# Performance work log

Measured on AMD Instinct MI355X. Metric: run time of the kernel, lower is better.

Reference implementation:

```python
import jax, jax.numpy as jnp
import numpy as np

NV, NK, DK, DV, KC = 32, 16, 128, 128, 4  # value heads, key heads, head dims, conv kernel
EPS = 1e-6


def setup_inputs() -> dict:
    key = jax.random.key(0)
    ks = jax.random.split(key, 10)
    B, T, D = 2, 4096, 2048
    key_dim, value_dim = NK * DK, NV * DV
    conv_dim = 2 * key_dim + value_dim
    s = 0.02
    return {
        "hidden_states": jax.random.normal(ks[0], (B, T, D), jnp.float32),
        "W_qkv": jax.random.normal(ks[1], (D, conv_dim), jnp.float32) * s,
        "W_z": jax.random.normal(ks[2], (D, value_dim), jnp.float32) * s,
        "W_b": jax.random.normal(ks[3], (D, NV), jnp.float32) * s,
        "W_a": jax.random.normal(ks[4], (D, NV), jnp.float32) * s,
        "conv_w": jax.random.normal(ks[5], (conv_dim, KC), jnp.float32) * 0.2,
        "dt_bias": jnp.ones((NV,), jnp.float32),
        "A_log": jnp.log(jax.random.uniform(ks[6], (NV,), jnp.float32, 0.5, 16.0)),
        "norm_w": jnp.ones((DV,), jnp.float32),
        "W_out": jax.random.normal(ks[7], (value_dim, D), jnp.float32) * s,
    }


def _silu(x):
    return x * jax.nn.sigmoid(x)


def _l2norm(x):
    return x * jax.lax.rsqrt(jnp.sum(x * x, axis=-1, keepdims=True) + EPS)


def _gated_delta_rule(q, k, v, g, beta):
    # q,k: [B,T,H,DK]; v: [B,T,H,DV]; g,beta: [B,T,H]
    tm = lambda x: jnp.moveaxis(x, 1, 0)  # time-major
    B, T, H = q.shape[0], q.shape[1], q.shape[2]
    S0 = jnp.zeros((B, H, q.shape[-1], v.shape[-1]), q.dtype)

    def step(S, xs):
        qt, kt, vt, gt, bt = xs
        S = S * jnp.exp(gt)[..., None, None]                       # decay
        kS = jnp.einsum('bhk,bhkv->bhv', kt, S)                    # k^T S
        S = S + bt[..., None, None] * kt[..., :, None] * (vt - kS)[..., None, :]
        o = jnp.einsum('bhk,bhkv->bhv', qt, S)
        return S, o

    _, o = jax.lax.scan(step, S0, (tm(q), tm(k), tm(v), tm(g), tm(beta)))
    return jnp.moveaxis(o, 0, 1)  # [B,T,H,DV]


def reference(hidden_states, W_qkv, W_z, W_b, W_a, conv_w, dt_bias, A_log, norm_w, W_out):
    B, T, D = hidden_states.shape
    key_dim, value_dim = NK * DK, NV * DV

    mixed = hidden_states @ W_qkv                                  # [B,T,conv_dim]
    z = (hidden_states @ W_z).reshape(B, T, NV, DV)
    beta = jax.nn.sigmoid(hidden_states @ W_b)                     # [B,T,NV]
    a = hidden_states @ W_a
    g = -jnp.exp(A_log) * jax.nn.softplus(a + dt_bias)             # [B,T,NV]

    # causal depthwise short conv (kernel KC) + silu
    xp = jnp.pad(mixed, ((0, 0), (KC - 1, 0), (0, 0)))
    conv = sum(xp[:, i:i + T, :] * conv_w[:, i] for i in range(KC))
    mixed = _silu(conv)

    q, k, v = jnp.split(mixed, [key_dim, 2 * key_dim], axis=-1)
    q = q.reshape(B, T, NK, DK)
    k = k.reshape(B, T, NK, DK)
    v = v.reshape(B, T, NV, DV)
    rep = NV // NK
    q = jnp.repeat(q, rep, axis=2)
    k = jnp.repeat(k, rep, axis=2)

    q = _l2norm(q) * (DK ** -0.5)
    k = _l2norm(k)

    o = _gated_delta_rule(q, k, v, g, beta)                        # [B,T,NV,DV]

    # fused gated RMSNorm: rmsnorm(o)*w * silu(z)
    var = jnp.mean(o * o, axis=-1, keepdims=True)
    o = o * jax.lax.rsqrt(var + 1e-6) * norm_w * _silu(z)

    return o.reshape(B, T, value_dim) @ W_out
```

## Files before the change

kernel.cpp:

```cpp
#include <hip/hip_runtime.h>
#include <hip/hip_bf16.h>


typedef __attribute__((ext_vector_type(8))) short short8;
typedef __attribute__((ext_vector_type(4))) float f32x4;
typedef unsigned short us;

static __device__ __forceinline__ us f2b(float f) {
  __hip_bfloat16 h = __float2bfloat16(f);
  return __builtin_bit_cast(us, h);
}
static __device__ __forceinline__ float b2f(us u) {
  return __bfloat162float(__builtin_bit_cast(__hip_bfloat16, u));
}
static __device__ __forceinline__ void bar_lds() {
  asm volatile("s_waitcnt lgkmcnt(0)" ::: "memory");
  __builtin_amdgcn_s_barrier();
}

__global__ __launch_bounds__(256) void cvt_f32_bf16(const float* __restrict__ in,
    us* __restrict__ out, long n4) {
  long i = (long)blockIdx.x * 256 + threadIdx.x;
  long stride = (long)gridDim.x * 256;
  for (; i < n4; i += stride) {
    float4 f = reinterpret_cast<const float4*>(in)[i];
    ushort4 u;
    u.x = f2b(f.x); u.y = f2b(f.y); u.z = f2b(f.z); u.w = f2b(f.w);
    reinterpret_cast<ushort4*>(out)[i] = u;
  }
}

__global__ __launch_bounds__(256) void transpose_cvt(const float* __restrict__ in,
    us* __restrict__ out, int K, int N, int Nfull, int coloff, int row_off) {
  __shared__ float tile[64][65];
  int tid = threadIdx.x;
  int n0 = blockIdx.x * 64, k0 = blockIdx.y * 64;
  int tx = tid & 15, ty = tid >> 4;
#pragma unroll
  for (int r = 0; r < 4; ++r) {
    int kk = k0 + ty + r * 16, nn = n0 + tx * 4;
    float4 v = make_float4(0.f, 0.f, 0.f, 0.f);
    if (kk < K && nn < N)
      v = *reinterpret_cast<const float4*>(in + (size_t)kk * Nfull + coloff + nn);
    tile[ty + r * 16][tx * 4 + 0] = v.x;
    tile[ty + r * 16][tx * 4 + 1] = v.y;
    tile[ty + r * 16][tx * 4 + 2] = v.z;
    tile[ty + r * 16][tx * 4 + 3] = v.w;
  }
  __syncthreads();
#pragma unroll
  for (int g = 0; g < 2; ++g) {
    int s = tid + g * 256;
    int nn = s >> 3, ks = (s & 7) * 8;
    if (n0 + nn < N && k0 + ks < K) {
      us ov[8];
#pragma unroll
      for (int i = 0; i < 8; ++i) ov[i] = f2b(tile[ks + i][nn]);
      *reinterpret_cast<uint4*>(out + (size_t)(n0 + nn + row_off) * K + k0 + ks) =
          *reinterpret_cast<uint4*>(ov);
    }
  }
}

template <bool BF16OUT>
__global__ __launch_bounds__(512, 1) void gemm256(const us* __restrict__ A,
    const us* __restrict__ B, void* __restrict__ Cout, int K, int ldC) {
  __shared__ us Abuf[2][256 * 64];
  __shared__ us Bbuf[2][256 * 64];
  int tid = threadIdx.x, w = tid >> 6, lane = tid & 63;
  int wr = w >> 2, wc = w & 3;
  int fr = lane & 15, j4 = lane >> 4;
  int lin = blockIdx.y * gridDim.x + blockIdx.x;
  int nwg = gridDim.x * gridDim.y;
  int wg = (lin & 7) * (nwg >> 3) + (lin >> 3);
  int bx = wg % gridDim.x, by = wg / gridDim.x;
  size_t bm = (size_t)bx * 256, bn = (size_t)by * 256;

  const us *aG[4], *bG[4];
  us *aL[2][4], *bL[2][4];
#pragma unroll
  for (int u = 0; u < 4; ++u) {
    int idx = u * 512 + tid;
    int row = idx >> 3, sl = idx & 7;
    int sg = (sl ^ (row & 7)) * 8;
    aG[u] = A + (bm + row) * K + sg;
    bG[u] = B + (bn + row) * K + sg;
    int lbase = (u * 64 + w * 8) * 64;
#pragma unroll
    for (int bf = 0; bf < 2; ++bf) {
      aL[bf][u] = &Abuf[bf][lbase];
      bL[bf][u] = &Bbuf[bf][lbase];
    }
  }

  f32x4 acc[8][4] = {};
#pragma unroll
  for (int u = 0; u < 4; ++u) {
    __builtin_amdgcn_global_load_lds((const void*)aG[u], (void*)aL[0][u], 16, 0, 0);
    __builtin_amdgcn_global_load_lds((const void*)bG[u], (void*)bL[0][u], 16, 0, 0);
  }
  __syncthreads();

  int nt = K >> 6;
  for (int t = 0; t < nt; ++t) {
    int cur = t & 1, nxt = cur ^ 1;
    const us* Ac = Abuf[cur];
    const us* Bc = Bbuf[cur];
    int kt1 = (t + 1) << 6;
    bool more = (t + 1 < nt);
#pragma unroll
    for (int q = 0; q < 4; ++q) {
      if (more) {
        __builtin_amdgcn_global_load_lds((const void*)(aG[q] + kt1), (void*)aL[nxt][q], 16, 0, 0);
        __builtin_amdgcn_global_load_lds((const void*)(bG[q] + kt1), (void*)bL[nxt][q], 16, 0, 0);
      }
      short8 a0[2], a1[2], bfv[4][2];
      int Ra0 = wr * 128 + 2 * q * 16 + fr;
      int Ra1 = Ra0 + 16;
#pragma unroll
      for (int ks = 0; ks < 2; ++ks) {
        a0[ks] = *reinterpret_cast<const short8*>(&Ac[Ra0 * 64 + (((ks * 4 + j4) ^ (Ra0 & 7)) * 8)]);
        a1[ks] = *reinterpret_cast<const short8*>(&Ac[Ra1 * 64 + (((ks * 4 + j4) ^ (Ra1 & 7)) * 8)]);
#pragma unroll
        for (int fj = 0; fj < 4; ++fj) {
          int Rb = wc * 64 + fj * 16 + fr;
          bfv[fj][ks] = *reinterpret_cast<const short8*>(&Bc[Rb * 64 + (((ks * 4 + j4) ^ (Rb & 7)) * 8)]);
        }
      }
      __builtin_amdgcn_s_setprio(1);
#pragma unroll
      for (int ks = 0; ks < 2; ++ks)
#pragma unroll
        for (int fj = 0; fj < 4; ++fj) {
          acc[2 * q][fj] = __builtin_amdgcn_mfma_f32_16x16x32_bf16(a0[ks], bfv[fj][ks], acc[2 * q][fj], 0, 0, 0);
          acc[2 * q + 1][fj] = __builtin_amdgcn_mfma_f32_16x16x32_bf16(a1[ks], bfv[fj][ks], acc[2 * q + 1][fj], 0, 0, 0);
        }
      __builtin_amdgcn_s_setprio(0);
    }
    __syncthreads();
  }
#pragma unroll
  for (int fi = 0; fi < 8; ++fi)
#pragma unroll
    for (int fj = 0; fj < 4; ++fj) {
      size_t col = bn + wc * 64 + fj * 16 + fr;
#pragma unroll
      for (int e = 0; e < 4; ++e) {
        size_t r = bm + wr * 128 + fi * 16 + j4 * 4 + e;
        size_t off = r * ldC + col;
        if (BF16OUT) reinterpret_cast<us*>(Cout)[off] = f2b(acc[fi][fj][e]);
        else reinterpret_cast<float*>(Cout)[off] = acc[fi][fj][e];
      }
    }
}

__global__ __launch_bounds__(256) void gemm_lds_f32(const us* __restrict__ A,
    const us* __restrict__ B, float* __restrict__ Cout,
    int K, int Nb1, int Nvalid, int ldC) {
  __shared__ us Ash[128 * 64];
  __shared__ us Bsh[128 * 64];
  int tid = threadIdx.x, w = tid >> 6, lane = tid & 63;
  int bm = blockIdx.x * 128, bn = blockIdx.y * 128;
  int wm = (w >> 1) * 64, wn = (w & 1) * 64;
  const us* aP[4]; const us* bP[4]; us* lA[4]; us* lB[4];
#pragma unroll
  for (int i = 0; i < 4; ++i) {
    int idx = i * 256 + tid;
    int row = idx >> 3;
    int sg = ((idx & 7) ^ (row & 7)) * 8;
    aP[i] = A + (size_t)(bm + row) * K + sg;
    int rb = bn + row; if (rb > Nb1) rb = Nb1;
    bP[i] = B + (size_t)rb * K + sg;
    lA[i] = &Ash[(i * 256 + w * 64) * 8];
    lB[i] = &Bsh[(i * 256 + w * 64) * 8];
  }
  f32x4 acc[4][4] = {};
  int fr = lane & 15, j = lane >> 4;
  for (int kt = 0; kt < K; kt += 64) {
#pragma unroll
    for (int i = 0; i < 4; ++i)
      __builtin_amdgcn_global_load_lds((const void*)(aP[i] + kt), (void*)lA[i], 16, 0, 0);
#pragma unroll
    for (int i = 0; i < 4; ++i)
      __builtin_amdgcn_global_load_lds((const void*)(bP[i] + kt), (void*)lB[i], 16, 0, 0);
    __syncthreads();
#pragma unroll
    for (int ks = 0; ks < 2; ++ks) {
      short8 af[4], bfr[4];
#pragma unroll
      for (int f = 0; f < 4; ++f) {
        int Ra = wm + f * 16 + fr;
        af[f] = *reinterpret_cast<const short8*>(&Ash[Ra * 64 + (((ks * 4 + j) ^ (Ra & 7)) * 8)]);
        int Rb = wn + f * 16 + fr;
        bfr[f] = *reinterpret_cast<const short8*>(&Bsh[Rb * 64 + (((ks * 4 + j) ^ (Rb & 7)) * 8)]);
      }
#pragma unroll
      for (int i = 0; i < 4; ++i)
#pragma unroll
        for (int jj = 0; jj < 4; ++jj)
          acc[i][jj] = __builtin_amdgcn_mfma_f32_16x16x32_bf16(af[i], bfr[jj], acc[i][jj], 0, 0, 0);
    }
    __syncthreads();
  }
#pragma unroll
  for (int i = 0; i < 4; ++i)
#pragma unroll
    for (int jj = 0; jj < 4; ++jj) {
      int c0 = bn + wn + jj * 16 + (lane & 15);
      if (c0 < Nvalid) {
#pragma unroll
        for (int e = 0; e < 4; ++e) {
          int r = bm + wm + i * 16 + (lane >> 4) * 4 + e;
          Cout[(size_t)r * ldC + c0] = acc[i][jj][e];
        }
      }
    }
}

template <int MODE>
__global__ __launch_bounds__(256) void conv_chunk(const us* __restrict__ mixed,
    const float* __restrict__ cw, us* __restrict__ outp, int headbase) {
  int bp = blockIdx.x, b = bp >> 10, tloc = (bp & 1023) * 4, tid = threadIdx.x;
  int c0 = tid * 8;
  float wv[8][4];
#pragma unroll
  for (int jj = 0; jj < 8; ++jj) {
    float4 w4 = *reinterpret_cast<const float4*>(cw + (size_t)(c0 + jj) * 4);
    wv[jj][0] = w4.x; wv[jj][1] = w4.y; wv[jj][2] = w4.z; wv[jj][3] = w4.w;
  }
  us rw[7][8];
#pragma unroll
  for (int i = 0; i < 7; ++i) {
    int tt = tloc - 3 + i;
    if (tt >= 0 && tt < 4096)
      *reinterpret_cast<uint4*>(rw[i]) = *reinterpret_cast<const uint4*>(
          mixed + ((size_t)(b * 4096 + tt)) * 2048 + c0);
    else
      *reinterpret_cast<uint4*>(rw[i]) = make_uint4(0, 0, 0, 0);
  }
  float x[4][8];
#pragma unroll
  for (int jj = 0; jj < 8; ++jj) {
#pragma unroll
    for (int tk = 0; tk < 4; ++tk) {
      float a = 0.f;
#pragma unroll
      for (int i = 0; i < 4; ++i) a += b2f(rw[tk + i][jj]) * wv[jj][i];
      x[tk][jj] = a / (1.f + __expf(-a));
    }
  }
  size_t bt0 = (size_t)b * 4096 + tloc;
  us ov[8];
  if (MODE < 2) {
    float s[4] = {};
#pragma unroll
    for (int tk = 0; tk < 4; ++tk) {
#pragma unroll
      for (int jj = 0; jj < 8; ++jj) s[tk] += x[tk][jj] * x[tk][jj];
    }
#pragma unroll
    for (int m = 1; m < 16; m <<= 1) {
#pragma unroll
      for (int tk = 0; tk < 4; ++tk) s[tk] += __shfl_xor(s[tk], m, 64);
    }
    const float sc = (MODE == 0 ? 0.08838834764831845f : 1.f);
    int head = tid >> 4, d0 = c0 & 127;
#pragma unroll
    for (int tk = 0; tk < 4; ++tk) {
      float rn = rsqrtf(s[tk] + 1e-6f) * sc;
#pragma unroll
      for (int jj = 0; jj < 8; ++jj) ov[jj] = f2b(x[tk][jj] * rn);
      *reinterpret_cast<uint4*>(outp + ((bt0 + tk) * 16 + head) * 128 + d0) =
          *reinterpret_cast<uint4*>(ov);
    }
  } else {
    int head = headbase + (c0 >> 7), d0 = c0 & 127;
#pragma unroll
    for (int tk = 0; tk < 4; ++tk) {
#pragma unroll
      for (int jj = 0; jj < 8; ++jj) ov[jj] = f2b(x[tk][jj]);
      *reinterpret_cast<uint4*>(outp + ((bt0 + tk) * 32 + head) * 128 + d0) =
          *reinterpret_cast<uint4*>(ov);
    }
  }
}

__global__ __launch_bounds__(256) void gates_cumsum(const float* __restrict__ ba,
    const float* __restrict__ dt_bias, const float* __restrict__ A_log,
    float* __restrict__ bl_g, float* __restrict__ beta_g) {
  int widx = blockIdx.x * 4 + (threadIdx.x >> 6);
  int lane = threadIdx.x & 63;
  int bh = widx >> 6, chunk = widx & 63;
  int b = bh >> 5, h = bh & 31;
  size_t btl = (size_t)b * 4096 + chunk * 64 + lane;
  float bv = ba[btl * 64 + h];
  float av = ba[btl * 64 + 32 + h];
  float beta = 1.f / (1.f + __expf(-bv));
  float xx = av + dt_bias[h];
  float sp = (xx > 20.f) ? xx : log1pf(__expf(xx));
  float g = -__expf(A_log[h]) * sp;
#pragma unroll
  for (int off = 1; off < 64; off <<= 1) {
    float n = __shfl_up(g, off, 64);
    if (lane >= off) g += n;
  }
  bl_g[(size_t)widx * 64 + lane] = g;
  beta_g[(size_t)widx * 64 + lane] = beta;
}

static __device__ __forceinline__ f32x4 tile_range(const us* A, int lda,
    const us* B, int ldb, int rt, int ct, int l0, int nk, int lane, f32x4 acc) {
  const us* ar = A + (rt * 16 + (lane & 15)) * lda + l0 * 16 + (lane >> 4) * 8;
  const us* br = B + (ct * 16 + (lane & 15)) * ldb + l0 * 16 + (lane >> 4) * 8;
#pragma unroll
  for (int ks = 0; ks < nk; ++ks) {
    short8 a = *reinterpret_cast<const short8*>(ar + ks * 32);
    short8 bb = *reinterpret_cast<const short8*>(br + ks * 32);
    acc = __builtin_amdgcn_mfma_f32_16x16x32_bf16(a, bb, acc, 0, 0, 0);
  }
  return acc;
}
template <int SA, int SB>
static __device__ __forceinline__ f32x4 tile_swz(const us* A, int lda,
    const us* B, int ldb, int rt, int ct, int nk, int lane, f32x4 acc) {
  int ra = rt * 16 + (lane & 15);
  int rb = ct * 16 + (lane & 15);
  int j = lane >> 4;
#pragma unroll
  for (int ks = 0; ks < nk; ++ks) {
    int slot = j + 4 * ks;
    int oa = (SA >= 0) ? ((slot ^ ((ra >> (SA < 0 ? 0 : SA)) & 7)) * 8) : (slot * 8);
    int ob = (SB >= 0) ? ((slot ^ ((rb >> (SB < 0 ? 0 : SB)) & 7)) * 8) : (slot * 8);
    short8 a = *reinterpret_cast<const short8*>(A + ra * lda + oa);
    short8 bb = *reinterpret_cast<const short8*>(B + rb * ldb + ob);
    acc = __builtin_amdgcn_mfma_f32_16x16x32_bf16(a, bb, acc, 0, 0, 0);
  }
  return acc;
}

__global__ __launch_bounds__(512, 1) void scan_p1(
    const us* __restrict__ k, const float* __restrict__ bl_g,
    const float* __restrict__ beta_g, us* __restrict__ Tg) {
  __shared__ us Kb[64 * 136];
  __shared__ us Ebt[64 * 72];
  __shared__ us W1[64 * 72], W1t[64 * 72], W3[64 * 72];
  __shared__ float bl_s[64], bet_s[64];
  us* const Eb = Kb;

  int bid = blockIdx.x, bh = bid >> 6, c = bid & 63;
  int b = bh >> 5, h = bh & 31, hk = h >> 1;
  int tid = threadIdx.x, w = tid >> 6, lane = tid & 63;
  int row = tid >> 3, c16 = (tid & 7) * 16;
  size_t bt0 = (size_t)b * 4096 + c * 64;

  const int TR_[10] = {0, 1, 1, 2, 2, 2, 3, 3, 3, 3};
  const int TC_[10] = {0, 0, 1, 0, 1, 2, 0, 1, 2, 3};

  const us* kp = k + ((bt0 + row) * 16 + hk) * 128 + c16;
  uint4 kr0 = reinterpret_cast<const uint4*>(kp)[0];
  uint4 kr1 = reinterpret_cast<const uint4*>(kp)[1];
  int gbase = (bh * 64 + c) * 64;
  if (tid < 64) { bl_s[tid] = bl_g[gbase + tid]; bet_s[tid] = beta_g[gbase + tid]; }
  *reinterpret_cast<uint4*>(&Kb[row * 136 + c16]) = kr0;
  *reinterpret_cast<uint4*>(&Kb[row * 136 + c16 + 8]) = kr1;
  __syncthreads();
  {
    int art = w & 3;
#pragma unroll
    for (int s = 0; s < 2; ++s) {
      int ct = (w >> 2) * 2 + s;
      f32x4 a = tile_range(Kb, 136, Kb, 136, art, ct, 0, 4, lane, f32x4{});
#pragma unroll
      for (int e = 0; e < 4; ++e) {
        int tr = art * 16 + (lane >> 4) * 4 + e;
        int cl = ct * 16 + (lane & 15);
        float dv = (cl < tr) ? bet_s[tr] * __expf(bl_s[tr] - bl_s[cl]) * a[e] : 0.f;
        W1[tr * 72 + cl] = f2b(dv);
        W1t[cl * 72 + tr] = f2b(dv);
        W3[tr * 72 + cl] = f2b((tr == cl ? 1.f : 0.f) - dv);
      }
    }
  }
  __syncthreads();
  f32x4 freg[2] = {};
#pragma unroll
  for (int it = 1; it <= 5; ++it) {
    if (it > 1) {
#pragma unroll
      for (int s = 0; s < 2; ++s) {
        int j = w + s * 8;
        if (j < 10) {
          int r = TR_[j], cc0 = TC_[j];
#pragma unroll
          for (int e = 0; e < 4; ++e) {
            int rr = r * 16 + (lane >> 4) * 4 + e, cl = cc0 * 16 + (lane & 15);
            W3[rr * 72 + cl] = f2b(b2f(W3[rr * 72 + cl]) + freg[s][e]);
          }
        }
      }
    }
    if (it == 1) {
      const int ZR[12] = {0, 0, 0, 1, 1, 2, 1, 2, 2, 3, 3, 3};
      const int ZC[12] = {1, 2, 3, 2, 3, 3, 0, 0, 1, 0, 1, 2};
#pragma unroll
      for (int u = 0; u < 12; ++u) {
        if ((u & 7) != w) continue;
        us* arr = (u < 6) ? Eb : Ebt;
        if (lane < 32) {
          int rr = ZR[u] * 16 + (lane >> 1);
          *reinterpret_cast<uint4*>(&arr[rr * 72 + ZC[u] * 16 + (lane & 1) * 8]) =
              make_uint4(0, 0, 0, 0);
        }
      }
    }
    const us* Es  = (it & 1) ? W1  : Eb;
    const us* Est = (it & 1) ? W1t : Ebt;
    us* Ed  = (it & 1) ? Eb  : W1;
    us* Edt = (it & 1) ? Ebt : W1t;
#pragma unroll
    for (int s = 0; s < 2; ++s) {
      int j = w + s * 8;
      if (j < 10) {
        int r = TR_[j], cc0 = TC_[j];
        int l0 = cc0 & ~1, nk = (r - l0 + 2) >> 1;
        f32x4 a = tile_range(Es, 72, Est, 72, r, cc0, l0, nk, lane, f32x4{});
#pragma unroll
        for (int e = 0; e < 4; ++e) {
          int rr = r * 16 + (lane >> 4) * 4 + e, cl = cc0 * 16 + (lane & 15);
          us val = f2b(a[e]);
          Ed[rr * 72 + cl] = val;
          Edt[cl * 72 + rr] = val;
        }
      }
    }
    __syncthreads();
    const us* Ent = (it & 1) ? Ebt : W1t;
#pragma unroll
    for (int s = 0; s < 2; ++s) {
      int j = w + s * 8;
      if (j < 10) {
        int r = TR_[j], cc0 = TC_[j];
        int l0 = cc0 & ~1, nk = (r - l0 + 2) >> 1;
        freg[s] = tile_range(W3, 72, Ent, 72, r, cc0, l0, nk, lane, f32x4{});
      }
    }
    __syncthreads();
  }
#pragma unroll
  for (int s = 0; s < 2; ++s) {
    int j = w + s * 8;
    if (j < 10) {
      int r = TR_[j], cc0 = TC_[j];
#pragma unroll
      for (int e = 0; e < 4; ++e) {
        int rr = r * 16 + (lane >> 4) * 4 + e, cl = cc0 * 16 + (lane & 15);
        W3[rr * 72 + cl] = f2b(b2f(W3[rr * 72 + cl]) + freg[s][e]);
      }
    }
  }
  __syncthreads();
  *reinterpret_cast<uint4*>(&Tg[(size_t)bid * 4096 + tid * 8]) =
      *reinterpret_cast<const uint4*>(&W3[row * 72 + (tid & 7) * 8]);
}

__global__ __launch_bounds__(512, 1) void scan_p2(
    const us* __restrict__ q, const us* __restrict__ k, const us* __restrict__ v,
    const float* __restrict__ bl_g, const float* __restrict__ beta_g,
    const us* __restrict__ Tg, us* __restrict__ o) {
  __shared__ us Sb[32 * 136];
  __shared__ us Kb[64 * 136];
  __shared__ us Qb[64 * 136];
  __shared__ us Ktb[128 * 72];
  __shared__ us Vt[32 * 72];
  __shared__ us Ut[32 * 72];
  __shared__ us W3[64 * 72];
  __shared__ us WP[64 * 72];
  __shared__ float bl_s[64], bet_s[64], ksc_s[64];

  int bid = blockIdx.x, vs = bid >> 6, bh = bid & 63;
  int b = bh >> 5, h = bh & 31, hk = h >> 1;
  int tid = threadIdx.x, w = tid >> 6, lane = tid & 63;
  int row = tid >> 3, c16 = (tid & 7) * 16;

  for (int i = tid; i < (32 * 136) / 8; i += 512)
    reinterpret_cast<uint4*>(Sb)[i] = make_uint4(0, 0, 0, 0);
  __syncthreads();

  uint4 kr0, kr1, qr0, qr1, vr, Tr;
  float blr, blC, bet, betv;
  int vrow = (tid & 255) >> 2, vseg = tid & 3;
  auto load_regs = [&](int c) {
    size_t bt0 = (size_t)b * 4096 + c * 64;
    const us* kp = k + ((bt0 + row) * 16 + hk) * 128 + c16;
    const us* qp = q + ((bt0 + row) * 16 + hk) * 128 + c16;
    kr0 = reinterpret_cast<const uint4*>(kp)[0];
    kr1 = reinterpret_cast<const uint4*>(kp)[1];
    qr0 = reinterpret_cast<const uint4*>(qp)[0];
    qr1 = reinterpret_cast<const uint4*>(qp)[1];
    Tr = *reinterpret_cast<const uint4*>(&Tg[((size_t)bh * 64 + c) * 4096 + tid * 8]);
    int gbase = (bh * 64 + c) * 64;
    blr = bl_g[gbase + row];
    blC = bl_g[gbase + 63];
    bet = beta_g[gbase + row];
    if (tid < 256) {
      vr = *reinterpret_cast<const uint4*>(
          v + ((bt0 + vrow) * 32 + h) * 128 + vs * 32 + vseg * 8);
      betv = beta_g[gbase + vrow];
    }
  };
  load_regs(0);

  for (int c = 0; c < 64; ++c) {
    size_t bt0 = (size_t)b * 4096 + c * 64;
    if ((tid & 7) == 0) {
      bl_s[row] = blr; bet_s[row] = bet;
      ksc_s[row] = __expf(blC - blr);
    }
    *reinterpret_cast<uint4*>(&Kb[row * 136 + c16]) = kr0;
    *reinterpret_cast<uint4*>(&Kb[row * 136 + c16 + 8]) = kr1;
    *reinterpret_cast<uint4*>(&Qb[row * 136 + c16]) = qr0;
    *reinterpret_cast<uint4*>(&Qb[row * 136 + c16 + 8]) = qr1;
    *reinterpret_cast<uint4*>(&W3[row * 72 + (tid & 7) * 8]) = Tr;
    if (tid < 256) {
      us vreg[8];
      *reinterpret_cast<uint4*>(vreg) = vr;
#pragma unroll
      for (int i = 0; i < 8; ++i) {
        int vv = vseg * 8 + i;
        Vt[vv * 72 + (((vrow >> 3) ^ vseg) & 7) * 8 + (vrow & 7)] = f2b(betv * b2f(vreg[i]));
      }
    }
    load_regs(c < 63 ? c + 1 : 63);
    bar_lds();
#pragma unroll
    for (int tk = 0; tk < 2; ++tk) {
      int task = tid + tk * 512;
      int d = task & 127, oct = task >> 7;
      us kt[8];
#pragma unroll
      for (int i = 0; i < 8; ++i)
        kt[i] = f2b(ksc_s[oct * 8 + i] * b2f(Kb[(oct * 8 + i) * 136 + d]));
      *reinterpret_cast<uint4*>(&Ktb[d * 72 + ((oct ^ ((d >> 4) & 7)) * 8)]) =
          *reinterpret_cast<uint4*>(kt);
    }
    int rtO = w >> 1, ctv = w & 1;
    f32x4 o1 = tile_swz<-1, -1>(Qb, 136, Sb, 136, rtO, ctv, 4, lane, f32x4{});
    {
      int art = w & 3;
#pragma unroll
      for (int s = 0; s < 2; ++s) {
        int ct = (w >> 2) * 2 + s;
        f32x4 a = tile_swz<-1, -1>(Qb, 136, Kb, 136, art, ct, 4, lane, f32x4{});
#pragma unroll
        for (int e = 0; e < 4; ++e) {
          int tr = art * 16 + (lane >> 4) * 4 + e;
          int cl = ct * 16 + (lane & 15);
          float pv = (cl <= tr) ? __expf(bl_s[tr] - bl_s[cl]) * a[e] : 0.f;
          WP[tr * 72 + cl] = f2b(pv);
        }
      }
    }
    {
      int vrt = w >> 2, ct = w & 3;
      f32x4 a = tile_swz<-1, -1>(Sb, 136, Kb, 136, vrt, ct, 4, lane, f32x4{});
      int tt = ct * 16 + (lane & 15);
      float csc = bet_s[tt] * __expf(bl_s[tt]);
#pragma unroll
      for (int e = 0; e < 4; ++e) {
        int vv = vrt * 16 + (lane >> 4) * 4 + e;
        int off = vv * 72 + (((tt >> 3) ^ ((vv >> 3) & 7)) * 8) + (tt & 7);
        Vt[off] = f2b(b2f(Vt[off]) - csc * a[e]);
      }
    }
    bar_lds();
    {
      int vrt = w >> 2, ct = w & 3;
      f32x4 a = tile_swz<3, -1>(Vt, 72, W3, 72, vrt, ct, 2, lane, f32x4{});
#pragma unroll
      for (int e = 0; e < 4; ++e) {
        int uv = vrt * 16 + (lane >> 4) * 4 + e;
        int ut2 = ct * 16 + (lane & 15);
        Ut[uv * 72 + (((ut2 >> 3) ^ ((uv >> 3) & 7)) * 8) + (ut2 & 7)] = f2b(a[e]);
      }
    }
    bar_lds();
    float lamC = __expf(bl_s[63]);
    {
      f32x4 a = tile_swz<-1, 3>(WP, 72, Ut, 72, rtO, ctv, 2, lane, f32x4{});
#pragma unroll
      for (int e = 0; e < 4; ++e) {
        int tt = rtO * 16 + (lane >> 4) * 4 + e;
        int vv = vs * 32 + ctv * 16 + (lane & 15);
        float val = __expf(bl_s[tt]) * o1[e] + a[e];
        o[((bt0 + tt) * 32 + h) * 128 + vv] = f2b(val);
      }
    }
#pragma unroll
    for (int s = 0; s < 2; ++s) {
      int ti = w * 2 + s;
      int vrt = ti >> 3, dt = ti & 7;
      f32x4 a = tile_swz<3, 4>(Ut, 72, Ktb, 72, vrt, dt, 2, lane, f32x4{});
#pragma unroll
      for (int e = 0; e < 4; ++e) {
        int vv = vrt * 16 + (lane >> 4) * 4 + e, dd = dt * 16 + (lane & 15);
        Sb[vv * 136 + dd] = f2b(lamC * b2f(Sb[vv * 136 + dd]) + a[e]);
      }
    }
    bar_lds();
  }
}

__global__ __launch_bounds__(256) void rms_gate(us* oy,
    const us* __restrict__ z, const float* __restrict__ nw) {
  int sub = threadIdx.x & 31;
  size_t row = (size_t)blockIdx.x * 8 + (threadIdx.x >> 5);
  size_t base = row * 128 + sub * 4;
  ushort4 ov = *reinterpret_cast<ushort4*>(oy + base);
  ushort4 zv = *reinterpret_cast<const ushort4*>(z + base);
  float o_[4] = {b2f(ov.x), b2f(ov.y), b2f(ov.z), b2f(ov.w)};
  float ss = o_[0] * o_[0] + o_[1] * o_[1] + o_[2] * o_[2] + o_[3] * o_[3];
#pragma unroll
  for (int m = 1; m < 32; m <<= 1) ss += __shfl_xor(ss, m, 64);
  float r = rsqrtf(ss * (1.f / 128.f) + 1e-6f);
  float4 w4 = *reinterpret_cast<const float4*>(nw + sub * 4);
  float zz[4] = {b2f(zv.x), b2f(zv.y), b2f(zv.z), b2f(zv.w)};
  float wv[4] = {w4.x, w4.y, w4.z, w4.w};
  us res[4];
#pragma unroll
  for (int i = 0; i < 4; ++i) {
    float zs = zz[i] / (1.f + __expf(-zz[i]));
    res[i] = f2b(o_[i] * r * wv[i] * zs);
  }
  *reinterpret_cast<ushort4*>(oy + base) = *reinterpret_cast<ushort4*>(res);
}

extern "C" void kernel_launch(void* const* d_in, const int* in_sizes, int n_in,
                              void* d_out, int out_size, void* d_ws, size_t ws_size,
                              hipStream_t stream) {
  const float* hs      = (const float*)d_in[0];
  const float* W_qkv   = (const float*)d_in[1];
  const float* W_z     = (const float*)d_in[2];
  const float* W_b     = (const float*)d_in[3];
  const float* W_a     = (const float*)d_in[4];
  const float* conv_w  = (const float*)d_in[5];
  const float* dt_bias = (const float*)d_in[6];
  const float* A_log   = (const float*)d_in[7];
  const float* norm_w  = (const float*)d_in[8];
  const float* W_out   = (const float*)d_in[9];
  float* out = (float*)d_out;

  char* ws = (char*)d_ws;
  const size_t MiB = 1u << 20;
  float* ba_buf = (float*)(ws);
  float* bl_g   = (float*)(ws + 2 * MiB);
  float* bt_g   = (float*)(ws + 3 * MiB);
  us*    wt     = (us*)(ws + 4 * MiB);
  us*    Tg     = (us*)(ws + 4 * MiB);
  us*    mixed  = (us*)(ws + 36 * MiB);
  us*    o_buf  = (us*)(ws + 36 * MiB);
  us*    hs_bf0 = (us*)(ws + 68 * MiB);
  us*    q_buf  = (us*)(ws + 100 * MiB);
  us*    hs_bf1 = q_buf;
  us*    k_buf  = (us*)(ws + 132 * MiB);
  us*    v_buf  = (us*)(ws + 164 * MiB);
  us*    z_bf   = v_buf;

  cvt_f32_bf16<<<2048, 256, 0, stream>>>(hs, hs_bf0, (long)8192 * 2048 / 4);

  for (int c = 0; c < 4; ++c) {
    transpose_cvt<<<dim3(32, 32), 256, 0, stream>>>(W_qkv, wt, 2048, 2048, 8192, c * 2048, 0);
    gemm256<true><<<dim3(32, 8), 512, 0, stream>>>(hs_bf0, wt, mixed, 2048, 2048);
    const float* cwc = conv_w + (size_t)c * 2048 * 4;
    if (c == 0)      conv_chunk<0><<<2048, 256, 0, stream>>>(mixed, cwc, q_buf, 0);
    else if (c == 1) conv_chunk<1><<<2048, 256, 0, stream>>>(mixed, cwc, k_buf, 0);
    else if (c == 2) conv_chunk<2><<<2048, 256, 0, stream>>>(mixed, cwc, v_buf, 0);
    else             conv_chunk<2><<<2048, 256, 0, stream>>>(mixed, cwc, v_buf, 16);
  }
  transpose_cvt<<<dim3(1, 32), 256, 0, stream>>>(W_b, wt, 2048, 32, 32, 0, 0);
  transpose_cvt<<<dim3(1, 32), 256, 0, stream>>>(W_a, wt, 2048, 32, 32, 0, 32);
  gemm_lds_f32<<<dim3(64, 1), 256, 0, stream>>>(hs_bf0, wt, ba_buf, 2048, 63, 64, 64);
  gates_cumsum<<<1024, 256, 0, stream>>>(ba_buf, dt_bias, A_log, bl_g, bt_g);
  scan_p1<<<4096, 512, 0, stream>>>(k_buf, bl_g, bt_g, Tg);
  scan_p2<<<256, 512, 0, stream>>>(q_buf, k_buf, v_buf, bl_g, bt_g, Tg, o_buf);
  cvt_f32_bf16<<<2048, 256, 0, stream>>>(hs, hs_bf1, (long)8192 * 2048 / 4);
  transpose_cvt<<<dim3(64, 32), 256, 0, stream>>>(W_z, wt, 2048, 4096, 4096, 0, 0);
  gemm256<true><<<dim3(32, 16), 512, 0, stream>>>(hs_bf1, wt, z_bf, 2048, 4096);
  rms_gate<<<32768, 256, 0, stream>>>(o_buf, z_bf, norm_w);
  transpose_cvt<<<dim3(32, 64), 256, 0, stream>>>(W_out, wt, 4096, 2048, 2048, 0, 0);
  gemm256<false><<<dim3(32, 8), 512, 0, stream>>>(o_buf, wt, out, 4096, 2048);
}
```

Measured before the change: 1.055 ms.

## Stage next scan chunk at loop tail and transpose W_qkv once

In scan_p2, the LDS staging of the next chunk's K, Q, W3, V and gate values now happens at the end of the current iteration, before its final barrier. This removes one block-wide barrier per chunk. The gate arrays are double-buffered so the next chunk's values can be written while the current ones are still being read. Separately, W_qkv is transposed and converted in a single launch instead of four, and the small W_b/W_a buffer moves to a separate region so it does not overwrite the full transposed weight.

```diff
diff --git a/kernel.cpp b/kernel.cpp
--- a/kernel.cpp
+++ b/kernel.cpp
@@ -475,7 +475,7 @@
   __shared__ us Ut[32 * 72];
   __shared__ us W3[64 * 72];
   __shared__ us WP[64 * 72];
-  __shared__ float bl_s[64], bet_s[64], ksc_s[64];
+  __shared__ float bl_s[2][64], bet_s[2][64], ksc_s[2][64];
 
   int bid = blockIdx.x, vs = bid >> 6, bh = bid & 63;
   int b = bh >> 5, h = bh & 31, hk = h >> 1;
@@ -484,7 +484,6 @@
 
   for (int i = tid; i < (32 * 136) / 8; i += 512)
     reinterpret_cast<uint4*>(Sb)[i] = make_uint4(0, 0, 0, 0);
-  __syncthreads();
 
   uint4 kr0, kr1, qr0, qr1, vr, Tr;
   float blr, blC, bet, betv;
@@ -508,13 +507,11 @@
       betv = beta_g[gbase + vrow];
     }
   };
-  load_regs(0);
-
-  for (int c = 0; c < 64; ++c) {
-    size_t bt0 = (size_t)b * 4096 + c * 64;
+  auto lf_write = [&](int cc) {
+    int pcw = cc & 1;
     if ((tid & 7) == 0) {
-      bl_s[row] = blr; bet_s[row] = bet;
-      ksc_s[row] = __expf(blC - blr);
+      bl_s[pcw][row] = blr; bet_s[pcw][row] = bet;
+      ksc_s[pcw][row] = __expf(blC - blr);
     }
     *reinterpret_cast<uint4*>(&Kb[row * 136 + c16]) = kr0;
     *reinterpret_cast<uint4*>(&Kb[row * 136 + c16 + 8]) = kr1;
@@ -530,8 +527,16 @@
         Vt[vv * 72 + (((vrow >> 3) ^ vseg) & 7) * 8 + (vrow & 7)] = f2b(betv * b2f(vreg[i]));
       }
     }
-    load_regs(c < 63 ? c + 1 : 63);
-    bar_lds();
+  };
+
+  load_regs(0);
+  lf_write(0);
+  load_regs(1);
+  bar_lds();
+
+  for (int c = 0; c < 64; ++c) {
+    int pc = c & 1;
+    size_t bt0 = (size_t)b * 4096 + c * 64;
 #pragma unroll
     for (int tk = 0; tk < 2; ++tk) {
       int task = tid + tk * 512;
@@ -539,7 +544,7 @@
       us kt[8];
 #pragma unroll
       for (int i = 0; i < 8; ++i)
-        kt[i] = f2b(ksc_s[oct * 8 + i] * b2f(Kb[(oct * 8 + i) * 136 + d]));
+        kt[i] = f2b(ksc_s[pc][oct * 8 + i] * b2f(Kb[(oct * 8 + i) * 136 + d]));
       *reinterpret_cast<uint4*>(&Ktb[d * 72 + ((oct ^ ((d >> 4) & 7)) * 8)]) =
           *reinterpret_cast<uint4*>(kt);
     }
@@ -555,7 +560,7 @@
         for (int e = 0; e < 4; ++e) {
           int tr = art * 16 + (lane >> 4) * 4 + e;
           int cl = ct * 16 + (lane & 15);
-          float pv = (cl <= tr) ? __expf(bl_s[tr] - bl_s[cl]) * a[e] : 0.f;
+          float pv = (cl <= tr) ? __expf(bl_s[pc][tr] - bl_s[pc][cl]) * a[e] : 0.f;
           WP[tr * 72 + cl] = f2b(pv);
         }
       }
@@ -564,7 +569,7 @@
       int vrt = w >> 2, ct = w & 3;
       f32x4 a = tile_swz<-1, -1>(Sb, 136, Kb, 136, vrt, ct, 4, lane, f32x4{});
       int tt = ct * 16 + (lane & 15);
-      float csc = bet_s[tt] * __expf(bl_s[tt]);
+      float csc = bet_s[pc][tt] * __expf(bl_s[pc][tt]);
 #pragma unroll
       for (int e = 0; e < 4; ++e) {
         int vv = vrt * 16 + (lane >> 4) * 4 + e;
@@ -584,14 +589,14 @@
       }
     }
     bar_lds();
-    float lamC = __expf(bl_s[63]);
+    float lamC = __expf(bl_s[pc][63]);
     {
       f32x4 a = tile_swz<-1, 3>(WP, 72, Ut, 72, rtO, ctv, 2, lane, f32x4{});
 #pragma unroll
       for (int e = 0; e < 4; ++e) {
         int tt = rtO * 16 + (lane >> 4) * 4 + e;
         int vv = vs * 32 + ctv * 16 + (lane & 15);
-        float val = __expf(bl_s[tt]) * o1[e] + a[e];
+        float val = __expf(bl_s[pc][tt]) * o1[e] + a[e];
         o[((bt0 + tt) * 32 + h) * 128 + vv] = f2b(val);
       }
     }
@@ -605,6 +610,10 @@
         int vv = vrt * 16 + (lane >> 4) * 4 + e, dd = dt * 16 + (lane & 15);
         Sb[vv * 136 + dd] = f2b(lamC * b2f(Sb[vv * 136 + dd]) + a[e]);
       }
+    }
+    if (c < 63) {
+      lf_write(c + 1);
+      load_regs(c + 2 <= 63 ? c + 2 : 63);
     }
     bar_lds();
   }
@@ -657,6 +666,7 @@
   us*    wt     = (us*)(ws + 4 * MiB);
   us*    Tg     = (us*)(ws + 4 * MiB);
   us*    mixed  = (us*)(ws + 36 * MiB);
+  us*    wt_sm  = (us*)(ws + 36 * MiB);
   us*    o_buf  = (us*)(ws + 36 * MiB);
   us*    hs_bf0 = (us*)(ws + 68 * MiB);
   us*    q_buf  = (us*)(ws + 100 * MiB);
@@ -667,18 +677,19 @@
 
   cvt_f32_bf16<<<2048, 256, 0, stream>>>(hs, hs_bf0, (long)8192 * 2048 / 4);
 
+  transpose_cvt<<<dim3(128, 32), 256, 0, stream>>>(W_qkv, wt, 2048, 8192, 8192, 0, 0);
   for (int c = 0; c < 4; ++c) {
-    transpose_cvt<<<dim3(32, 32), 256, 0, stream>>>(W_qkv, wt, 2048, 2048, 8192, c * 2048, 0);
-    gemm256<true><<<dim3(32, 8), 512, 0, stream>>>(hs_bf0, wt, mixed, 2048, 2048);
+    gemm256<true><<<dim3(32, 8), 512, 0, stream>>>(
+        hs_bf0, wt + (size_t)c * 2048 * 2048, mixed, 2048, 2048);
     const float* cwc = conv_w + (size_t)c * 2048 * 4;
     if (c == 0)      conv_chunk<0><<<2048, 256, 0, stream>>>(mixed, cwc, q_buf, 0);
     else if (c == 1) conv_chunk<1><<<2048, 256, 0, stream>>>(mixed, cwc, k_buf, 0);
     else if (c == 2) conv_chunk<2><<<2048, 256, 0, stream>>>(mixed, cwc, v_buf, 0);
     else             conv_chunk<2><<<2048, 256, 0, stream>>>(mixed, cwc, v_buf, 16);
   }
-  transpose_cvt<<<dim3(1, 32), 256, 0, stream>>>(W_b, wt, 2048, 32, 32, 0, 0);
-  transpose_cvt<<<dim3(1, 32), 256, 0, stream>>>(W_a, wt, 2048, 32, 32, 0, 32);
-  gemm_lds_f32<<<dim3(64, 1), 256, 0, stream>>>(hs_bf0, wt, ba_buf, 2048, 63, 64, 64);
+  transpose_cvt<<<dim3(1, 32), 256, 0, stream>>>(W_b, wt_sm, 2048, 32, 32, 0, 0);
+  transpose_cvt<<<dim3(1, 32), 256, 0, stream>>>(W_a, wt_sm, 2048, 32, 32, 0, 32);
+  gemm_lds_f32<<<dim3(64, 1), 256, 0, stream>>>(hs_bf0, wt_sm, ba_buf, 2048, 63, 64, 64);
   gates_cumsum<<<1024, 256, 0, stream>>>(ba_buf, dt_bias, A_log, bl_g, bt_g);
   scan_p1<<<4096, 512, 0, stream>>>(k_buf, bl_g, bt_g, Tg);
   scan_p2<<<256, 512, 0, stream>>>(q_buf, k_buf, v_buf, bl_g, bt_g, Tg, o_buf);
```

Result: no change. 1.051 ms (-0.3%).
